# Kernel optimization log

Hardware: AMD Instinct MI355X
Metric: run time of the kernel (lower is better)

The kernel has to match this reference:

```python
import jax, jax.numpy as jnp
import numpy as np
from jax import lax

S, B, I, H, L, O, T = 128, 64, 1024, 1024, 2, 1024, 64


def lstm_cell(x, h, c, wih, whh, b):
    # PyTorch gate order: i, f, g, o
    g = x @ wih.T + h @ whh.T + b  # [B, 4H]
    i, f, gg, o = jnp.split(g, 4, axis=-1)
    c = jax.nn.sigmoid(f) * c + jax.nn.sigmoid(i) * jnp.tanh(gg)
    h = jax.nn.sigmoid(o) * jnp.tanh(c)
    return h, c


def run_lstm_seq(xs, wih, whh, b):
    # xs: [S, B, in]; zero initial state (torch default)
    h0 = jnp.zeros((xs.shape[1], whh.shape[-1]), xs.dtype)

    def step(carry, x):
        h, c = lstm_cell(x, carry[0], carry[1], wih, whh, b)
        return (h, c), h

    (h, c), ys = lax.scan(step, (h0, h0), xs)
    return ys, h, c


def setup_inputs() -> dict:
    key = jax.random.key(0)
    ks = jax.random.split(key, 10)
    s = 1.0 / np.sqrt(H)
    u = lambda k, shape: jax.random.uniform(k, shape, minval=-s, maxval=s, dtype=jnp.float32)
    return {
        "input_seq": jax.random.normal(ks[0], (S, B, I), dtype=jnp.float32),
        "enc_wih": u(ks[1], (L, 4 * H, I)),
        "enc_whh": u(ks[2], (L, 4 * H, H)),
        "enc_b": u(ks[3], (L, 4 * H)),
        "dec_wih": u(ks[4], (L, 4 * H, I)),
        "dec_whh": u(ks[5], (L, 4 * H, H)),
        "dec_b": u(ks[6], (L, 4 * H)),
        "lin_w": u(ks[7], (O, H)),
        "lin_b": u(ks[8], (O,)),
        "target_seq_length": T,
    }


def reference(input_seq, enc_wih, enc_whh, enc_b, dec_wih, dec_whh, dec_b, lin_w, lin_b, target_seq_length):
    # ---- encoder: stacked LSTM over the full sequence ----
    xs = input_seq
    hs, cs = [], []
    for l in range(L):
        xs, h, c = run_lstm_seq(xs, enc_wih[l], enc_whh[l], enc_b[l])
        hs.append(h)
        cs.append(c)
    hs = jnp.stack(hs)  # [L, B, H]
    cs = jnp.stack(cs)

    x0 = input_seq[-1]  # [B, I]

    def dec_step(carry, _):
        x, hs, cs = carry
        inp = x
        nh, nc = [], []
        for l in range(L):
            h, c = lstm_cell(inp, hs[l], cs[l], dec_wih[l], dec_whh[l], dec_b[l])
            nh.append(h)
            nc.append(c)
            inp = h
        y = inp @ lin_w.T + lin_b  # [B, O]
        return (y, jnp.stack(nh), jnp.stack(nc)), y

    _, outs = lax.scan(dec_step, (x0, hs, cs), None, length=target_seq_length)
    return jnp.transpose(outs, (1, 0, 2))  # [B, T, O]
```

## Files before the change

### kernel.cpp

```cpp
#include <hip/hip_runtime.h>
#include <math.h>


typedef unsigned short u16;
typedef short short8 __attribute__((ext_vector_type(8)));
typedef float f32x4 __attribute__((ext_vector_type(4)));

#define MFMA_BF16 __builtin_amdgcn_mfma_f32_16x16x32_bf16

__device__ __forceinline__ u16 f2bf(float x) {
  unsigned u = __builtin_bit_cast(unsigned, x);
  unsigned r = u + 0x7fffu + ((u >> 16) & 1u);
  return (u16)(r >> 16);
}
__device__ __forceinline__ float bf2f(u16 b) {
  return __builtin_bit_cast(float, ((unsigned)b) << 16);
}
__device__ __forceinline__ int permrow(int r) {
  int gate = r >> 10, hc = r & 1023;
  return ((hc >> 2) << 4) + ((hc & 3) << 2) + gate;
}

__device__ __forceinline__ void st_sc(u16* p, u16 v) {
  unsigned vv = v;
  asm volatile("global_store_short %0, %1, off sc0 sc1" :: "v"(p), "v"(vv) : "memory");
}
__device__ __forceinline__ int coh_load(const int* p) {
  int v;
  asm volatile("global_load_dword %0, %1, off sc0 sc1\n\ts_waitcnt vmcnt(0)"
               : "=v"(v) : "v"(p) : "memory");
  return v;
}
__device__ __forceinline__ void coh_store(int* p, int v) {
  asm volatile("global_store_dword %0, %1, off sc0 sc1\n\ts_waitcnt vmcnt(0)"
               :: "v"(p), "v"(v) : "memory");
}


__global__ void split_mat(const float* __restrict__ src, u16* __restrict__ dh,
                          u16* __restrict__ dl, int n, int mode) {
  int i = blockIdx.x * 256 + threadIdx.x;
  if (i >= n) return;
  float v = src[i];
  u16 hi = f2bf(v);
  u16 lo = f2bf(v - bf2f(hi));
  int r = i >> 10, c = i & 1023;
  int idx = i;
  if (mode == 1) idx = c * 1024 + r;
  else if (mode == 2) idx = permrow(r) * 1024 + c;
  dh[idx] = hi; dl[idx] = lo;
}

__global__ void zero_f4(float4* __restrict__ p, int n) {
  int i = blockIdx.x * 256 + threadIdx.x;
  if (i < n) p[i] = make_float4(0.f, 0.f, 0.f, 0.f);
}

__global__ void bias_perm(const float* __restrict__ in, float* __restrict__ out) {
  int i = blockIdx.x * 256 + threadIdx.x;
  if (i < 4096) out[permrow(i)] = in[i];
}

__global__ void bias_comb(const float* __restrict__ db0, const float* __restrict__ lb,
                          const float* __restrict__ wih, float* __restrict__ out) {
  __shared__ float red[256];
  int n = blockIdx.x;
  float s = 0.f;
  for (int k = threadIdx.x; k < 1024; k += 256) s += lb[k] * wih[(size_t)n * 1024 + k];
  red[threadIdx.x] = s;
  __syncthreads();
  for (int d = 128; d > 0; d >>= 1) {
    if (threadIdx.x < d) red[threadIdx.x] += red[threadIdx.x + d];
    __syncthreads();
  }
  if (threadIdx.x == 0) out[permrow(n)] = db0[n] + red[0];
}

template<int MT>
__global__ __launch_bounds__(256) void gemm_split(
    const u16* __restrict__ Ah, const u16* __restrict__ Al, int lda,
    const u16* __restrict__ Bh, const u16* __restrict__ Bl, int ldb,
    int K, int gn,
    u16* __restrict__ Ch, u16* __restrict__ Cl, int ldc,
    float* __restrict__ outp, const float* __restrict__ bias, int ldout, int mode) {
  int bm = blockIdx.x / gn, bn = blockIdx.x % gn;
  int l = threadIdx.x & 63, w = threadIdx.x >> 6;
  int n0 = bn * 128 + w * 32;
  int rr = l & 15, ko = (l >> 4) << 3, q = l >> 4;
  int M0 = bm * 64 * MT;
  f32x4 acc[8 * MT] = {};
  for (int kk = 0; kk < K; kk += 32) {
    short8 bh[2], bl[2];
#pragma unroll
    for (int nt = 0; nt < 2; ++nt) {
      size_t bo = (size_t)(n0 + nt * 16 + rr) * ldb + kk + ko;
      bh[nt] = *(const short8*)(Bh + bo);
      bl[nt] = *(const short8*)(Bl + bo);
    }
#pragma unroll
    for (int mt = 0; mt < 4 * MT; ++mt) {
      size_t ao = (size_t)(M0 + mt * 16 + rr) * lda + kk + ko;
      short8 ah = *(const short8*)(Ah + ao);
      short8 al = *(const short8*)(Al + ao);
#pragma unroll
      for (int nt = 0; nt < 2; ++nt) {
        f32x4 t = acc[mt * 2 + nt];
        t = MFMA_BF16(ah, bh[nt], t, 0, 0, 0);
        t = MFMA_BF16(ah, bl[nt], t, 0, 0, 0);
        t = MFMA_BF16(al, bh[nt], t, 0, 0, 0);
        acc[mt * 2 + nt] = t;
      }
    }
  }
#pragma unroll
  for (int mt = 0; mt < 4 * MT; ++mt)
#pragma unroll
    for (int nt = 0; nt < 2; ++nt)
#pragma unroll
      for (int r = 0; r < 4; ++r) {
        int row = M0 + mt * 16 + q * 4 + r;
        int col = n0 + nt * 16 + rr;
        float v = acc[mt * 2 + nt][r];
        if (mode == 0) {
          u16 hh = f2bf(v);
          Ch[(size_t)row * ldc + col] = hh;
          Cl[(size_t)row * ldc + col] = f2bf(v - bf2f(hh));
        } else if (mode == 1) {
          int t = row >> 6, b = row & 63;
          outp[(size_t)b * 65536 + t * 1024 + col] = v + bias[col];
        } else {
          outp[(size_t)row * ldout + col] = v;
        }
      }
}


struct Half {
  const u16 *Ah, *Al, *Wh, *Wl;
  const float* pre;
  const float* bias;
  float* c;
  u16 *Hh, *Hl;
  int active;
};

__global__ __launch_bounds__(512, 1) void lstm_pair(Half hA, Half hB) {
  int j = blockIdx.x;
  Half S = (j < 128) ? hA : hB;
  if (!S.active) return;
  int sub = j & 127;
  int rowblk = ((sub & 7) << 4) | (sub >> 3);
  int R = rowblk << 5;
  int tid = threadIdx.x;
  int l = tid & 63, w = tid >> 6;
  int rr = l & 15, ko = (l >> 4) << 3, q = l >> 4;
  int kb = w << 7;
  const u16* __restrict__ Wh = S.Wh + (size_t)(R + rr) * 1024 + kb + ko;
  const u16* __restrict__ Wl = S.Wl + (size_t)(R + rr) * 1024 + kb + ko;
  const u16* __restrict__ Ah = S.Ah + kb + ko;
  const u16* __restrict__ Al = S.Al + kb + ko;

  f32x4 acc[8] = {};
#pragma unroll
  for (int kk = 0; kk < 128; kk += 32) {
    short8 bh[2], bl[2];
#pragma unroll
    for (int nt = 0; nt < 2; ++nt) {
      bh[nt] = *(const short8*)(Wh + (size_t)(nt << 4) * 1024 + kk);
      bl[nt] = *(const short8*)(Wl + (size_t)(nt << 4) * 1024 + kk);
    }
#pragma unroll
    for (int mt = 0; mt < 4; ++mt) {
      size_t ao = (size_t)((mt << 4) + rr) * 1024 + kk;
      short8 ah = *(const short8*)(Ah + ao);
      short8 al = *(const short8*)(Al + ao);
#pragma unroll
      for (int nt = 0; nt < 2; ++nt) {
        f32x4 t = acc[mt * 2 + nt];
        t = MFMA_BF16(ah, bh[nt], t, 0, 0, 0);
        t = MFMA_BF16(ah, bl[nt], t, 0, 0, 0);
        t = MFMA_BF16(al, bh[nt], t, 0, 0, 0);
        acc[mt * 2 + nt] = t;
      }
    }
  }

  __shared__ float lds[8][64][33];
#pragma unroll
  for (int mt = 0; mt < 4; ++mt)
#pragma unroll
    for (int nt = 0; nt < 2; ++nt)
#pragma unroll
      for (int r = 0; r < 4; ++r)
        lds[w][(mt << 4) + (q << 2) + r][(nt << 4) + rr] = acc[mt * 2 + nt][r];
  __syncthreads();

  int b = tid >> 3, e = tid & 7;
  float g[4];
#pragma unroll
  for (int gt = 0; gt < 4; ++gt) {
    int c = (e << 2) + gt;
    float s = S.bias[R + c] + S.pre[(size_t)b * 4096 + R + c];
#pragma unroll
    for (int ww = 0; ww < 8; ++ww) s += lds[ww][b][c];
    g[gt] = s;
  }
  int hc = (rowblk << 3) + e;
  size_t ci = (size_t)b * 1024 + hc;
  float cold = S.c[ci];
  float is = 1.f / (1.f + expf(-g[0]));
  float fs = 1.f / (1.f + expf(-g[1]));
  float gg = tanhf(g[2]);
  float os = 1.f / (1.f + expf(-g[3]));
  float cn = fs * cold + is * gg;
  S.c[ci] = cn;
  float h = os * tanhf(cn);
  S.Hh[ci] = f2bf(h);
  S.Hl[ci] = f2bf(h - bf2f(f2bf(h)));
}


struct DecL {
  const u16 *W00h, *W00l;
  const u16 *W01h, *W01l;
  const u16 *W10h, *W10l;
  const u16 *W11h, *W11l;
  const u16 *h0i_h, *h0i_l;
  const u16 *h1i_h, *h1i_l;
  const u16 *zh, *zl;
  const float *Gd0, *dbp0, *bdec0, *dbp1;
  const float *c0, *c1;
  u16 *D0h, *D0l;
  u16 *H1h, *H1l;
  int* bar;
};

__global__ __launch_bounds__(512, 1) void lstm_dec_layers(DecL D) {
  int j = blockIdx.x;
  int lay = j >> 7;
  int sub = j & 127;
  int rowblk = ((sub & 7) << 4) | (sub >> 3);
  int R = rowblk << 5;
  int tid = threadIdx.x;
  int l = tid & 63, w = tid >> 6;
  int rr = l & 15, ko = (l >> 4) << 3, q = l >> 4;
  int opidx = w >> 2;
  int kb = (w & 3) << 8;
  int* flagA = D.bar;
  int* flagB = D.bar + 2048;

  const u16* Wh_ = lay ? (opidx ? D.W11h : D.W10h) : (opidx ? D.W01h : D.W00h);
  const u16* Wl_ = lay ? (opidx ? D.W11l : D.W10l) : (opidx ? D.W01l : D.W00l);
  short8 wh[2][8], wl[2][8];
#pragma unroll
  for (int nt = 0; nt < 2; ++nt)
#pragma unroll
    for (int ki = 0; ki < 8; ++ki) {
      size_t o = (size_t)(R + (nt << 4) + rr) * 1024 + kb + (ki << 5) + ko;
      wh[nt][ki] = *(const short8*)(Wh_ + o);
      wl[nt][ki] = *(const short8*)(Wl_ + o);
    }

  int b = tid >> 3, e = tid & 7;
  int hc = (rowblk << 3) + e;
  size_t ci = (size_t)b * 1024 + hc;
  float creg = lay ? D.c1[ci] : D.c0[ci];
  float bT[4], gb0[4];
#pragma unroll
  for (int gt = 0; gt < 4; ++gt) {
    int cc = R + (e << 2) + gt;
    bT[gt] = lay ? D.dbp1[cc] : D.bdec0[cc];
    gb0[gt] = lay ? 0.f : (D.dbp0[cc] + D.Gd0[(size_t)b * 4096 + cc]);
  }

  __shared__ float lds[8][64][33];

  for (int t = 0; t < 64; ++t) {
    if (lay) {
      if (tid < 128) {
        const int* p = flagA + (tid << 4);
        while (coh_load(p) < t + 1) __builtin_amdgcn_s_sleep(4);
      }
    } else if (t > 0) {
      if (tid < 128) {
        const int* p = flagB + (tid << 4);
        while (coh_load(p) < t) __builtin_amdgcn_s_sleep(4);
      }
    }
    __syncthreads();

    const u16 *Aph, *Apl;
    if (!lay) {
      if (opidx == 0) {
        Aph = t ? D.H1h + (size_t)(t - 1) * 65536 : D.zh;
        Apl = t ? D.H1l + (size_t)(t - 1) * 65536 : D.zl;
      } else {
        Aph = t ? D.D0h + (size_t)(t - 1) * 65536 : D.h0i_h;
        Apl = t ? D.D0l + (size_t)(t - 1) * 65536 : D.h0i_l;
      }
    } else {
      if (opidx == 0) {
        Aph = D.D0h + (size_t)t * 65536;
        Apl = D.D0l + (size_t)t * 65536;
      } else {
        Aph = t ? D.H1h + (size_t)(t - 1) * 65536 : D.h1i_h;
        Apl = t ? D.H1l + (size_t)(t - 1) * 65536 : D.h1i_l;
      }
    }
    const u16* __restrict__ Ah_ = Aph + kb + ko;
    const u16* __restrict__ Al_ = Apl + kb + ko;

    f32x4 acc[8] = {};
#pragma unroll
    for (int ki = 0; ki < 8; ++ki) {
#pragma unroll
      for (int mt = 0; mt < 4; ++mt) {
        size_t ao = (size_t)((mt << 4) + rr) * 1024 + (ki << 5);
        short8 ah = *(const short8*)(Ah_ + ao);
        short8 al = *(const short8*)(Al_ + ao);
#pragma unroll
        for (int nt = 0; nt < 2; ++nt) {
          f32x4 tacc = acc[mt * 2 + nt];
          tacc = MFMA_BF16(ah, wh[nt][ki], tacc, 0, 0, 0);
          tacc = MFMA_BF16(ah, wl[nt][ki], tacc, 0, 0, 0);
          tacc = MFMA_BF16(al, wh[nt][ki], tacc, 0, 0, 0);
          acc[mt * 2 + nt] = tacc;
        }
      }
    }
#pragma unroll
    for (int mt = 0; mt < 4; ++mt)
#pragma unroll
      for (int nt = 0; nt < 2; ++nt)
#pragma unroll
        for (int r = 0; r < 4; ++r)
          lds[w][(mt << 4) + (q << 2) + r][(nt << 4) + rr] = acc[mt * 2 + nt][r];
    __syncthreads();

    float g[4];
#pragma unroll
    for (int gt = 0; gt < 4; ++gt) {
      int c = (e << 2) + gt;
      float s = (!lay && t == 0) ? gb0[gt] : bT[gt];
#pragma unroll
      for (int ww = 0; ww < 8; ++ww) s += lds[ww][b][c];
      g[gt] = s;
    }
    float is = 1.f / (1.f + expf(-g[0]));
    float fs = 1.f / (1.f + expf(-g[1]));
    float gg = tanhf(g[2]);
    float os = 1.f / (1.f + expf(-g[3]));
    float cn = fs * creg + is * gg;
    creg = cn;
    float h = os * tanhf(cn);
    u16 hh = f2bf(h), hl = f2bf(h - bf2f(hh));
    size_t oidx = (size_t)t * 65536 + ci;
    if (!lay) { st_sc(D.D0h + oidx, hh); st_sc(D.D0l + oidx, hl); }
    else      { st_sc(D.H1h + oidx, hh); st_sc(D.H1l + oidx, hl); }
    __syncthreads();
    if (tid == 0) coh_store((lay ? flagB : flagA) + (sub << 4), t + 1);
  }
}


extern "C" void kernel_launch(void* const* d_in, const int* in_sizes, int n_in,
                              void* d_out, int out_size, void* d_ws, size_t ws_size,
                              hipStream_t stream) {
  (void)in_sizes; (void)n_in; (void)out_size; (void)ws_size;
  const float* input_seq = (const float*)d_in[0];
  const float* enc_wih   = (const float*)d_in[1];
  const float* enc_whh   = (const float*)d_in[2];
  const float* enc_b     = (const float*)d_in[3];
  const float* dec_wih   = (const float*)d_in[4];
  const float* dec_whh   = (const float*)d_in[5];
  const float* dec_b     = (const float*)d_in[6];
  const float* lin_w     = (const float*)d_in[7];
  const float* lin_b     = (const float*)d_in[8];
  float* out = (float*)d_out;

  const size_t WE = 4096ull * 1024;
  const size_t HB = 64ull * 1024;
  char* ws = (char*)d_ws;
  size_t off = 0;
  auto alloc16 = [&](size_t elems) {
    u16* p = (u16*)(ws + off);
    off = (off + elems * 2 + 255) & ~(size_t)255;
    return p;
  };
  auto allocf = [&](size_t elems) {
    float* p = (float*)(ws + off);
    off = (off + elems * 4 + 255) & ~(size_t)255;
    return p;
  };

  u16 *WihE0h = alloc16(WE), *WihE0l = alloc16(WE);
  u16 *WhhE0h = alloc16(WE), *WhhE0l = alloc16(WE);
  u16 *WihE1h = alloc16(WE), *WihE1l = alloc16(WE);
  u16 *WhhE1h = alloc16(WE), *WhhE1l = alloc16(WE);
  u16 *WihD0h = alloc16(WE), *WihD0l = alloc16(WE);
  u16 *WhhD0h = alloc16(WE), *WhhD0l = alloc16(WE);
  u16 *WihD1h = alloc16(WE), *WihD1l = alloc16(WE);
  u16 *WhhD1h = alloc16(WE), *WhhD1l = alloc16(WE);
  u16 *Wcombh = alloc16(WE), *Wcombl = alloc16(WE);
  u16 *WLh  = alloc16(1024 * 1024), *WLl  = alloc16(1024 * 1024);
  u16 *WLTh = alloc16(1024 * 1024), *WLTl = alloc16(1024 * 1024);
  u16 *XCh = alloc16(16 * HB), *XCl = alloc16(16 * HB);
  u16 *XLh = alloc16(HB), *XLl = alloc16(HB);
  u16 *H0ch = alloc16(17 * HB), *H0cl = alloc16(17 * HB);
  u16 *H1h = alloc16(64 * HB), *H1l = alloc16(64 * HB);
  u16 *D0h = alloc16(64 * HB), *D0l = alloc16(64 * HB);
  size_t zbeg = off;
  u16 *zh = alloc16(HB), *zl = alloc16(HB);
  float *c0 = allocf(HB), *c1 = allocf(HB);
  int *barbuf = (int*)(ws + off);
  off = (off + 4096 * sizeof(int) + 255) & ~(size_t)255;
  size_t zend = off;
  u16 *e1h = alloc16(2 * HB), *e1l = alloc16(2 * HB);
  float *G0 = allocf(1024ull * 4096);
  float *G1 = allocf(1024ull * 4096);
  float *Gd0 = allocf(64 * 4096);
  float *ebp0 = allocf(4096), *ebp1 = allocf(4096);
  float *dbp0 = allocf(4096), *dbp1 = allocf(4096);
  float *bdec0 = allocf(4096);

  {
    int n4 = (int)((zend - zbeg) / 16);
    zero_f4<<<dim3((n4 + 255) / 256), dim3(256), 0, stream>>>((float4*)(ws + zbeg), n4);
  }
  auto split = [&](const float* src, u16* dh, u16* dl, int n, int mode) {
    split_mat<<<dim3((n + 255) / 256), dim3(256), 0, stream>>>(src, dh, dl, n, mode);
  };
  split(enc_wih,        WihE0h, WihE0l, (int)WE, 2);
  split(enc_whh,        WhhE0h, WhhE0l, (int)WE, 2);
  split(enc_wih + WE,   WihE1h, WihE1l, (int)WE, 2);
  split(enc_whh + WE,   WhhE1h, WhhE1l, (int)WE, 2);
  split(dec_wih,        WihD0h, WihD0l, (int)WE, 2);
  split(dec_whh,        WhhD0h, WhhD0l, (int)WE, 2);
  split(dec_wih + WE,   WihD1h, WihD1l, (int)WE, 2);
  split(dec_whh + WE,   WhhD1h, WhhD1l, (int)WE, 2);
  split(lin_w, WLh,  WLl,  1024 * 1024, 0);
  split(lin_w, WLTh, WLTl, 1024 * 1024, 1);
  split(input_seq + 127ull * HB, XLh, XLl, (int)HB, 0);
  bias_perm<<<dim3(16), dim3(256), 0, stream>>>(enc_b,        ebp0);
  bias_perm<<<dim3(16), dim3(256), 0, stream>>>(enc_b + 4096, ebp1);
  bias_perm<<<dim3(16), dim3(256), 0, stream>>>(dec_b,        dbp0);
  bias_perm<<<dim3(16), dim3(256), 0, stream>>>(dec_b + 4096, dbp1);
  bias_comb<<<dim3(4096), dim3(256), 0, stream>>>(dec_b, lin_b, dec_wih, bdec0);
  gemm_split<2><<<dim3(32 * 8), dim3(256), 0, stream>>>(
      WihD0h, WihD0l, 1024, WLTh, WLTl, 1024, 1024, 8,
      Wcombh, Wcombl, 1024, nullptr, nullptr, 0, 0);
  gemm_split<1><<<dim3(32), dim3(256), 0, stream>>>(
      XLh, XLl, 1024, WihD0h, WihD0l, 1024, 1024, 32,
      nullptr, nullptr, 0, Gd0, nullptr, 4096, 2);

  for (int ch = 0; ch < 8; ++ch) {
    split(input_seq + (size_t)ch * 16 * HB, XCh, XCl, (int)(16 * HB), 0);
    gemm_split<2><<<dim3(8 * 32), dim3(256), 0, stream>>>(
        XCh, XCl, 1024, WihE0h, WihE0l, 1024, 1024, 32,
        nullptr, nullptr, 0, G0, nullptr, 4096, 2);
    for (int lt = 0; lt < 16; ++lt) {
      int t0 = ch * 16 + lt;
      int t1 = (ch - 1) * 16 + lt;
      Half A;
      A.Ah = (t0 == 0) ? zh : (lt == 0 ? H0ch + 16ull * HB : H0ch + (size_t)lt * HB);
      A.Al = (t0 == 0) ? zl : (lt == 0 ? H0cl + 16ull * HB : H0cl + (size_t)lt * HB);
      A.Wh = WhhE0h; A.Wl = WhhE0l;
      A.pre = G0 + (size_t)lt * 64 * 4096;
      A.bias = ebp0; A.c = c0;
      A.Hh = H0ch + (size_t)(lt + 1) * HB; A.Hl = H0cl + (size_t)(lt + 1) * HB;
      A.active = 1;
      Half B;
      B.Ah = (t1 == 0) ? zh : e1h + (size_t)((t1 - 1) & 1) * HB;
      B.Al = (t1 == 0) ? zl : e1l + (size_t)((t1 - 1) & 1) * HB;
      B.Wh = WhhE1h; B.Wl = WhhE1l;
      B.pre = G1 + (size_t)lt * 64 * 4096;
      B.bias = ebp1; B.c = c1;
      B.Hh = e1h + (size_t)((t1 >= 0 ? t1 : 0) & 1) * HB;
      B.Hl = e1l + (size_t)((t1 >= 0 ? t1 : 0) & 1) * HB;
      B.active = (ch >= 1) ? 1 : 0;
      lstm_pair<<<dim3(256), dim3(512), 0, stream>>>(A, B);
    }
    gemm_split<2><<<dim3(8 * 32), dim3(256), 0, stream>>>(
        H0ch + HB, H0cl + HB, 1024, WihE1h, WihE1l, 1024, 1024, 32,
        nullptr, nullptr, 0, G1, nullptr, 4096, 2);
  }
  for (int lt = 0; lt < 16; ++lt) {
    int t1 = 112 + lt;
    Half A; A.active = 0;
    A.Ah = zh; A.Al = zl; A.Wh = WhhE0h; A.Wl = WhhE0l;
    A.pre = G0; A.bias = ebp0; A.c = c0; A.Hh = H0ch; A.Hl = H0cl;
    Half B;
    B.Ah = e1h + (size_t)((t1 - 1) & 1) * HB;
    B.Al = e1l + (size_t)((t1 - 1) & 1) * HB;
    B.Wh = WhhE1h; B.Wl = WhhE1l;
    B.pre = G1 + (size_t)lt * 64 * 4096;
    B.bias = ebp1; B.c = c1;
    B.Hh = e1h + (size_t)(t1 & 1) * HB;
    B.Hl = e1l + (size_t)(t1 & 1) * HB;
    B.active = 1;
    lstm_pair<<<dim3(256), dim3(512), 0, stream>>>(A, B);
  }

  {
    DecL P;
    P.W00h = Wcombh; P.W00l = Wcombl;
    P.W01h = WhhD0h; P.W01l = WhhD0l;
    P.W10h = WihD1h; P.W10l = WihD1l;
    P.W11h = WhhD1h; P.W11l = WhhD1l;
    P.h0i_h = H0ch + 16ull * HB; P.h0i_l = H0cl + 16ull * HB;
    P.h1i_h = e1h + HB; P.h1i_l = e1l + HB;
    P.zh = zh; P.zl = zl;
    P.Gd0 = Gd0; P.dbp0 = dbp0; P.bdec0 = bdec0; P.dbp1 = dbp1;
    P.c0 = c0; P.c1 = c1;
    P.D0h = D0h; P.D0l = D0l;
    P.H1h = H1h; P.H1l = H1l;
    P.bar = barbuf;
    lstm_dec_layers<<<dim3(256), dim3(512), 0, stream>>>(P);
  }

  gemm_split<2><<<dim3(32 * 8), dim3(256), 0, stream>>>(
      H1h, H1l, 1024, WLh, WLl, 1024, 1024, 8,
      nullptr, nullptr, 0, out, lin_b, 1024, 1);
}
```

Measured before the change: 6.441 ms.

## Per-wave flag polling by operand dependency and double-buffered A-operand loads in decoder

Replaces the block-wide flag spin (128 threads then __syncthreads) with per-wave polling, where each wave waits only on the flag its operand actually depends on. Waves using the recurrent or already-available operand can start their MFMAs earlier. Also software-pipelines the A-tile global loads with two register buffers so the next k-slice loads overlap the current MFMAs. The sleep interval is shortened, which means more polling traffic. Removing the barrier is valid only if the later LDS __syncthreads still orders everything correctly.

```diff
diff --git a/kernel.cpp b/kernel.cpp
--- a/kernel.cpp
+++ b/kernel.cpp
@@ -34,6 +34,13 @@
 __device__ __forceinline__ void coh_store(int* p, int v) {
   asm volatile("global_store_dword %0, %1, off sc0 sc1\n\ts_waitcnt vmcnt(0)"
                :: "v"(p), "v"(v) : "memory");
+}
+
+__device__ __forceinline__ void wave_wait(const int* fl, int need, int l) {
+  const int* p1 = fl + (l << 4);
+  while (coh_load(p1) < need) __builtin_amdgcn_s_sleep(1);
+  const int* p2 = fl + ((l + 64) << 4);
+  while (coh_load(p2) < need) __builtin_amdgcn_s_sleep(1);
 }
 
 
@@ -235,6 +242,26 @@
   int* bar;
 };
 
+#define LOADK(AH, AL, KI)                                              \
+  _Pragma("unroll")                                                    \
+  for (int mt = 0; mt < 4; ++mt) {                                     \
+    size_t ao = (size_t)((mt << 4) + rr) * 1024 + ((KI) << 5);         \
+    AH[mt] = *(const short8*)(Ah_ + ao);                               \
+    AL[mt] = *(const short8*)(Al_ + ao);                               \
+  }
+#define MFMAK(AH, AL, KI)                                              \
+  _Pragma("unroll")                                                    \
+  for (int mt = 0; mt < 4; ++mt) {                                     \
+    _Pragma("unroll")                                                  \
+    for (int nt = 0; nt < 2; ++nt) {                                   \
+      f32x4 tacc = acc[mt * 2 + nt];                                   \
+      tacc = MFMA_BF16(AH[mt], wh[nt][KI], tacc, 0, 0, 0);             \
+      tacc = MFMA_BF16(AH[mt], wl[nt][KI], tacc, 0, 0, 0);             \
+      tacc = MFMA_BF16(AL[mt], wh[nt][KI], tacc, 0, 0, 0);             \
+      acc[mt * 2 + nt] = tacc;                                         \
+    }                                                                  \
+  }
+
 __global__ __launch_bounds__(512, 1) void lstm_dec_layers(DecL D) {
   int j = blockIdx.x;
   int lay = j >> 7;
@@ -276,18 +303,12 @@
   __shared__ float lds[8][64][33];
 
   for (int t = 0; t < 64; ++t) {
-    if (lay) {
-      if (tid < 128) {
-        const int* p = flagA + (tid << 4);
-        while (coh_load(p) < t + 1) __builtin_amdgcn_s_sleep(4);
-      }
-    } else if (t > 0) {
-      if (tid < 128) {
-        const int* p = flagB + (tid << 4);
-        while (coh_load(p) < t) __builtin_amdgcn_s_sleep(4);
-      }
-    }
-    __syncthreads();
+    if (opidx == 1) {
+      if (t > 0) wave_wait(lay ? flagB : flagA, t, l);
+    } else {
+      if (lay)            wave_wait(flagA, t + 1, l);
+      else if (t > 0)     wave_wait(flagB, t, l);
+    }
 
     const u16 *Aph, *Apl;
     if (!lay) {
@@ -311,22 +332,24 @@
     const u16* __restrict__ Al_ = Apl + kb + ko;
 
     f32x4 acc[8] = {};
-#pragma unroll
-    for (int ki = 0; ki < 8; ++ki) {
-#pragma unroll
-      for (int mt = 0; mt < 4; ++mt) {
-        size_t ao = (size_t)((mt << 4) + rr) * 1024 + (ki << 5);
-        short8 ah = *(const short8*)(Ah_ + ao);
-        short8 al = *(const short8*)(Al_ + ao);
-#pragma unroll
-        for (int nt = 0; nt < 2; ++nt) {
-          f32x4 tacc = acc[mt * 2 + nt];
-          tacc = MFMA_BF16(ah, wh[nt][ki], tacc, 0, 0, 0);
-          tacc = MFMA_BF16(ah, wl[nt][ki], tacc, 0, 0, 0);
-          tacc = MFMA_BF16(al, wh[nt][ki], tacc, 0, 0, 0);
-          acc[mt * 2 + nt] = tacc;
-        }
-      }
+    {
+      short8 xah[4], xal[4], yah[4], yal[4];
+      LOADK(xah, xal, 0)
+      LOADK(yah, yal, 1)
+      MFMAK(xah, xal, 0)
+      LOADK(xah, xal, 2)
+      MFMAK(yah, yal, 1)
+      LOADK(yah, yal, 3)
+      MFMAK(xah, xal, 2)
+      LOADK(xah, xal, 4)
+      MFMAK(yah, yal, 3)
+      LOADK(yah, yal, 5)
+      MFMAK(xah, xal, 4)
+      LOADK(xah, xal, 6)
+      MFMAK(yah, yal, 5)
+      LOADK(yah, yal, 7)
+      MFMAK(xah, xal, 6)
+      MFMAK(yah, yal, 7)
     }
 #pragma unroll
     for (int mt = 0; mt < 4; ++mt)
```

Measured after the change: 6.127 ms. -4.9%, faster.
